# Optimization experiments

Measured on AMD Instinct MI355X. Metric: run time of the kernel, lower is better.

The kernel has to match this reference:

```python
import jax, jax.numpy as jnp
import numpy as np

SR = 44100
S_TAUS = [10.0, 50.0, 100.0]   # ms
L_TAUS = [500.0, 1500.0, 3000.0]  # ms
EPS = 1e-8


def ms2coef(ms, sr):
    return float(1.0 - np.exp(-2200.0 / (ms * sr)))


def ema(x, coef):
    # First-order leaky integrator y[t] = coef*x[t] + (1-coef)*y[t-1], y[-1]=0.
    # x: [B, T]; scan over time with carry of shape [B].
    coef = jnp.asarray(coef, x.dtype)
    one_m = jnp.asarray(1.0, x.dtype) - coef

    def step(carry, xt):
        y = coef * xt + one_m * carry
        return y, y

    _, ys = jax.lax.scan(step, jnp.zeros(x.shape[0], x.dtype), x.T)
    return ys.T  # [B, T]


def hadamard(x):
    # mid/side transform on channel dim (-2), orthonormal scaling
    m = x[..., 0, :] + x[..., 1, :]
    s = x[..., 0, :] - x[..., 1, :]
    return jnp.stack([m, s], axis=-2) * jnp.asarray(np.sqrt(0.5), x.dtype)


def ldr_feat(x_sq, s_coef, l_coef, shift):
    # log short-term envelope minus (time-aligned) log long-term envelope
    short = jnp.log(ema(x_sq, s_coef))
    long_ = jnp.log(ema(x_sq, l_coef))
    return short - jnp.roll(long_, -shift, axis=-1)


def setup_inputs() -> dict:
    key = jax.random.key(0)
    k1, k2 = jax.random.split(key)
    x_pred = jax.random.normal(k1, (4, 2, 1048576), dtype=jnp.float32)
    x_true = jax.random.normal(k2, (4, 2, 1048576), dtype=jnp.float32)
    return {"x_pred": x_pred, "x_true": x_true}


def reference(x_pred, x_true):
    xp = hadamard(x_pred)
    xt = hadamard(x_true)
    T = xp.shape[-1]
    ps = jnp.clip(jnp.square(xp), EPS, None).reshape(-1, T)
    ts = jnp.clip(jnp.square(xt), EPS, None).reshape(-1, T)
    total = jnp.asarray(0.0, x_pred.dtype)
    for s_ms, l_ms in zip(S_TAUS, L_TAUS):
        sc = ms2coef(s_ms, SR)
        lc = ms2coef(l_ms, SR)
        shift = int(SR * (l_ms - s_ms) * 0.0005)
        fp = ldr_feat(ps, sc, lc, shift)
        ft = ldr_feat(ts, sc, lc, shift)
        total = total + jnp.mean(jnp.abs(fp - ft))
    return total
```

## Files before the change

### kernel.cpp

```cpp
#include <hip/hip_runtime.h>
#include <cmath>


#define T_LEN    1048576
#define CHUNKS   256
#define CLEN     4096
#define NT1      256
#define SEG1     16
#define COLS     65536
#define JMAX     65535
#define EPS_CLIP 1e-8f
#define K2SEG    32
#define K2NSEG   8

struct K1Args {
  float d[6];
  float apw[6][7];
};
struct K2Args {
  float dL[6];
  float dL32[6];
};
struct CarryPack {
  float d[3];
  float apw[3][9];
};

__device__ __constant__ const int D_SHIFT[3] = {10804, 31972, 63945};

__global__ __launch_bounds__(NT1)
void k1_stage(const float* __restrict__ xp, const float* __restrict__ xt,
              float* __restrict__ Eloc, float* __restrict__ Bs,
              float* __restrict__ Bl, int mode, K1Args ka)
{
  int chunk = blockIdx.x, b = blockIdx.y;
  int which = b >> 2, sig = b & 3, tid = threadIdx.x;
  long base = (long)chunk * CLEN + (long)tid * SEG1;
  const float* x0 = (which ? xt : xp) + (long)sig * 2 * T_LEN;
  const float* x1 = x0 + T_LEN;

  float S[12];
#pragma unroll
  for (int j = 0; j < 12; j++) S[j] = 0.f;

#pragma unroll
  for (int i = 0; i < SEG1 / 4; i++) {
    float4 a = *(const float4*)(x0 + base + 4*i);
    float4 c4 = *(const float4*)(x1 + base + 4*i);
    float sm, sp, pm, ps;
#define STEP(CMP) \
    sm = a.CMP + c4.CMP; sp = a.CMP - c4.CMP; \
    pm = fmaxf(0.5f * sm * sm, EPS_CLIP); ps = fmaxf(0.5f * sp * sp, EPS_CLIP); \
    _Pragma("unroll") \
    for (int cf = 0; cf < 6; cf++) { \
      S[cf*2+0] = fmaf(ka.d[cf], S[cf*2+0], pm); \
      S[cf*2+1] = fmaf(ka.d[cf], S[cf*2+1], ps); \
    }
    STEP(x) STEP(y) STEP(z) STEP(w)
#undef STEP
  }

  int lane = tid & 63, w = tid >> 6;
#pragma unroll
  for (int i = 0; i < 6; i++) {
#pragma unroll
    for (int j = 0; j < 12; j++) {
      float up = __shfl_up(S[j], 1u << i, 64);
      if (lane >= (1 << i)) S[j] = fmaf(ka.apw[j >> 1][i], up, S[j]);
    }
  }
  __shared__ float WT[4][12];
  if (lane == 63)
#pragma unroll
    for (int j = 0; j < 12; j++) WT[w][j] = S[j];
  __syncthreads();
  float C[12];
#pragma unroll
  for (int j = 0; j < 12; j++) C[j] = 0.f;
#pragma unroll
  for (int i = 0; i < 4; i++) {
    if (i < w) {
#pragma unroll
      for (int j = 0; j < 12; j++)
        C[j] = fmaf(ka.apw[j >> 1][6], C[j], WT[i][j]);
    }
  }
  float alp[6];
#pragma unroll
  for (int cf = 0; cf < 6; cf++) {
    int e = lane + 1;
    float a = 1.f;
#pragma unroll
    for (int i = 0; i < 7; i++)
      if (e & (1 << i)) a *= ka.apw[cf][i];
    alp[cf] = a;
  }
#pragma unroll
  for (int j = 0; j < 12; j++) S[j] = fmaf(alp[j >> 1], C[j], S[j]);

  long col = (long)chunk * (CLEN / SEG1) + tid;
  if (mode & 2) {
#pragma unroll
    for (int k = 0; k < 3; k++)
#pragma unroll
      for (int st2 = 0; st2 < 2; st2++)
        Bs[(long)(4*k + which*2 + st2) * (4L*COLS) + (long)sig*COLS + col] = S[4*k + st2];
  }
  if (mode & 1) {
#pragma unroll
    for (int k = 0; k < 3; k++)
#pragma unroll
      for (int st2 = 0; st2 < 2; st2++)
        Bl[(long)(4*k + which*2 + st2) * (4L*COLS) + (long)sig*COLS + col] = S[4*k + 2 + st2];
  }
  if (mode != 2 && tid == NT1 - 1) {
#pragma unroll
    for (int cf = 0; cf < 6; cf++)
#pragma unroll
      for (int st = 0; st < 2; st++)
        Eloc[chunk * 96 + (which*8 + sig*2 + st) * 6 + cf] = S[cf*2 + st];
  }
}

__global__ __launch_bounds__(768)
void k2_scan(const float* __restrict__ Eloc, float* __restrict__ Y, K2Args ka,
             float* __restrict__ out)
{
  int col = threadIdx.x;
  int seg = threadIdx.y;
  if (col == 0 && seg == 0) out[0] = 0.f;
  float dL = ka.dL[col % 6];
  float A  = ka.dL32[col % 6];
  int c0 = seg * K2SEG;

  float yloc[K2SEG];
  float y = 0.f;
#pragma unroll
  for (int i = 0; i < K2SEG; i++) {
    y = fmaf(dL, y, Eloc[(c0 + i) * 96 + col]);
    yloc[i] = y;
  }
  __shared__ float SY[K2NSEG][96];
  SY[seg][col] = y;
  __syncthreads();
  float C = 0.f;
  for (int s = 0; s < seg; s++) C = fmaf(A, C, SY[s][col]);
  float w = dL;
#pragma unroll
  for (int i = 0; i < K2SEG; i++) {
    Y[(c0 + i) * 96 + col] = fmaf(w, C, yloc[i]);
    w *= dL;
  }
}

__global__ __launch_bounds__(256)
void k3_table(const float* __restrict__ Bl, const float* __restrict__ Y,
              float* __restrict__ Etab, CarryPack cp)
{
  int chunk = blockIdx.x, sig = blockIdx.y, tid = threadIdx.x;
  long col = (long)chunk * 256 + tid;

  float Yc[12];
#pragma unroll
  for (int j = 0; j < 12; j++) Yc[j] = 0.f;
  if (chunk > 0) {
    const float* Yp = Y + (chunk - 1) * 96;
    int rm = sig * 2;
#pragma unroll
    for (int k = 0; k < 3; k++) {
      int cf = 2*k + 1;
      Yc[4*k+0] = Yp[rm*6 + cf];       Yc[4*k+1] = Yp[(rm+1)*6 + cf];
      Yc[4*k+2] = Yp[(8+rm)*6 + cf];   Yc[4*k+3] = Yp[(8+rm+1)*6 + cf];
    }
  }
  float fac[3];
#pragma unroll
  for (int k = 0; k < 3; k++) {
    int e = tid + 1;
    float a = 1.f;
#pragma unroll
    for (int i = 0; i < 9; i++)
      if (e & (1 << i)) a *= cp.apw[k][i];
    fac[k] = a;
  }
#pragma unroll
  for (int k = 0; k < 3; k++) {
    float y0 = fmaf(fac[k], Yc[4*k+0], Bl[(long)(4*k+0)*(4L*COLS) + (long)sig*COLS + col]);
    float y1 = fmaf(fac[k], Yc[4*k+1], Bl[(long)(4*k+1)*(4L*COLS) + (long)sig*COLS + col]);
    float y2 = fmaf(fac[k], Yc[4*k+2], Bl[(long)(4*k+2)*(4L*COLS) + (long)sig*COLS + col]);
    float y3 = fmaf(fac[k], Yc[4*k+3], Bl[(long)(4*k+3)*(4L*COLS) + (long)sig*COLS + col]);
    float em = __log2f(y0) - __log2f(y2);
    float es = __log2f(y1) - __log2f(y3);
    long rowm = (long)(k*8 + sig*2);
    Etab[rowm * COLS + col] = em;
    Etab[(rowm+1) * COLS + col] = es;
  }
}

__device__ __forceinline__ float slow_lerp(const float* __restrict__ row, int q)
{
  int qm = q - 15;
  if (qm < 0) return row[0];
  int j = qm >> 4;
  if (j >= JMAX) return row[JMAX];
  float f = (float)(qm & 15) * 0.0625f;
  float a = row[j], b = row[j + 1];
  return fmaf(f, b - a, a);
}

__global__ __launch_bounds__(256)
void k4all(const float* __restrict__ xp, const float* __restrict__ xt,
           const float* __restrict__ Y, const float* __restrict__ Bs,
           const float* __restrict__ Etab, CarryPack cp, float* __restrict__ out)
{
  int chunk = blockIdx.x, sig = blockIdx.y, tid = threadIdx.x;
  long col = (long)chunk * 256 + tid;
  long base = col * 16;

  float Yc[12];
#pragma unroll
  for (int j = 0; j < 12; j++) Yc[j] = 0.f;
  if (chunk > 0) {
    const float* Yp = Y + (chunk - 1) * 96;
    int rm = sig * 2;
#pragma unroll
    for (int k = 0; k < 3; k++) {
      int cf = 2*k;
      Yc[4*k+0] = Yp[rm*6 + cf];       Yc[4*k+1] = Yp[(rm+1)*6 + cf];
      Yc[4*k+2] = Yp[(8+rm)*6 + cf];   Yc[4*k+3] = Yp[(8+rm+1)*6 + cf];
    }
  }
  float y[12];
  if (tid == 0) {
#pragma unroll
    for (int j = 0; j < 12; j++) y[j] = Yc[j];
  } else {
    float fac[3];
#pragma unroll
    for (int k = 0; k < 3; k++) {
      float a = 1.f;
#pragma unroll
      for (int i = 0; i < 8; i++)
        if (tid & (1 << i)) a *= cp.apw[k][i];
      fac[k] = a;
    }
#pragma unroll
    for (int k = 0; k < 3; k++)
#pragma unroll
      for (int q = 0; q < 4; q++)
        y[4*k+q] = fmaf(fac[k], Yc[4*k+q],
                        Bs[(long)(4*k+q)*(4L*COLS) + (long)sig*COLS + (col-1)]);
  }

  float tm0[3], tm1[3], tm2[3], ts0[3], ts1[3], ts2[3];
  int ofs[3], q0a[3]; bool fastp[3];
#pragma unroll
  for (int k = 0; k < 3; k++) {
    int q0 = (int)base + D_SHIFT[k]; if (q0 >= T_LEN) q0 -= T_LEN;
    q0a[k] = q0;
    int qm = q0 - 15;
    bool f = (qm >= 0) && ((qm >> 4) <= JMAX - 2);
    fastp[k] = f;
    const float* Tm = Etab + (long)(k * 8 + sig * 2) * COLS;
    const float* Ts = Tm + COLS;
    int j0 = f ? (qm >> 4) : 0;
    ofs[k] = f ? (qm & 15) : 0;
    tm0[k] = Tm[j0]; tm1[k] = Tm[j0 + 1]; tm2[k] = Tm[j0 + 2];
    ts0[k] = Ts[j0]; ts1[k] = Ts[j0 + 1]; ts2[k] = Ts[j0 + 2];
  }

  const float* p0 = xp + (long)sig * 2 * T_LEN;
  const float* p1 = p0 + T_LEN;
  const float* t0 = xt + (long)sig * 2 * T_LEN;
  const float* t1 = t0 + T_LEN;

  float acc0 = 0.f, acc1 = 0.f;
#pragma unroll
  for (int qt = 0; qt < 4; qt++) {
    float4 a4 = *(const float4*)(p0 + base + 4*qt);
    float4 b4 = *(const float4*)(p1 + base + 4*qt);
    float4 u4 = *(const float4*)(t0 + base + 4*qt);
    float4 w4 = *(const float4*)(t1 + base + 4*qt);
#define SAMP(CI, CMP) { \
      const int m = 4*qt + CI; \
      float sm = a4.CMP + b4.CMP, sd = a4.CMP - b4.CMP; \
      float pm = fmaxf(0.5f*sm*sm, EPS_CLIP), ps = fmaxf(0.5f*sd*sd, EPS_CLIP); \
      float em_ = u4.CMP + w4.CMP, ed_ = u4.CMP - w4.CMP; \
      float qm_ = fmaxf(0.5f*em_*em_, EPS_CLIP), qs_ = fmaxf(0.5f*ed_*ed_, EPS_CLIP); \
      _Pragma("unroll") \
      for (int k = 0; k < 3; k++) { \
        float dd = cp.d[k]; \
        y[4*k+0] = fmaf(dd, y[4*k+0], pm);  y[4*k+1] = fmaf(dd, y[4*k+1], ps); \
        y[4*k+2] = fmaf(dd, y[4*k+2], qm_); y[4*k+3] = fmaf(dd, y[4*k+3], qs_); \
        float Dm = __log2f(y[4*k+0]) - __log2f(y[4*k+2]); \
        float Ds = __log2f(y[4*k+1]) - __log2f(y[4*k+3]); \
        float em, es; \
        if (fastp[k]) { \
          int d0 = ofs[k] + m; \
          bool hi = d0 >= 16; \
          float am = hi ? tm1[k] : tm0[k], bm = hi ? tm2[k] : tm1[k]; \
          float as = hi ? ts1[k] : ts0[k], bs = hi ? ts2[k] : ts1[k]; \
          float f = (float)(d0 - (hi ? 16 : 0)) * 0.0625f; \
          em = fmaf(f, bm - am, am); \
          es = fmaf(f, bs - as, as); \
        } else { \
          int q = q0a[k] + m; if (q >= T_LEN) q -= T_LEN; \
          const float* Tm = Etab + (long)(k * 8 + sig * 2) * COLS; \
          em = slow_lerp(Tm, q); \
          es = slow_lerp(Tm + COLS, q); \
        } \
        acc0 += fabsf(Dm - em); \
        acc1 += fabsf(Ds - es); \
      } \
    }
    SAMP(0,x) SAMP(1,y) SAMP(2,z) SAMP(3,w)
#undef SAMP
  }

  float acc = acc0 + acc1;
#pragma unroll
  for (int off = 32; off > 0; off >>= 1) acc += __shfl_down(acc, off, 64);
  __shared__ float psum[4];
  int lane = tid & 63, w = tid >> 6;
  if (lane == 0) psum[w] = acc;
  __syncthreads();
  if (tid == 0) {
    const float SCALE = (float)(0.6931471805599453 / (8.0 * 1048576.0));
    float s = psum[0] + psum[1] + psum[2] + psum[3];
    atomicAdd(out, s * SCALE);
  }
}

extern "C" void kernel_launch(void* const* d_in, const int* in_sizes, int n_in,
                              void* d_out, int out_size, void* d_ws, size_t ws_size,
                              hipStream_t stream)
{
  (void)in_sizes; (void)n_in; (void)out_size;
  const float* xp = (const float*)d_in[0];
  const float* xt = (const float*)d_in[1];
  float* out = (float*)d_out;
  char* ws = (char*)d_ws;

  const size_t OFF_ELOC = 0;
  const size_t OFF_Y    = 98304;
  const size_t OFF_ETAB = 212992;
  const size_t OFF_B    = 6504448;
  const size_t HALF_B   = 12L * 4 * COLS * 4;
  const size_t NEED_FULL = OFF_B + 2 * HALF_B;
  float* Eloc = (float*)(ws + OFF_ELOC);
  float* Ybuf = (float*)(ws + OFF_Y);
  float* Etab = (float*)(ws + OFF_ETAB);
  float* Bsh  = (float*)(ws + OFF_B);
  float* Blo  = (float*)(ws + OFF_B + HALF_B);

  static const double S_MS[3] = {10.0, 50.0, 100.0};
  static const double L_MS[3] = {500.0, 1500.0, 3000.0};

  K1Args k1a; K2Args k2a; CarryPack cpS, cpL;
  for (int k = 0; k < 3; k++) {
    for (int which = 0; which < 2; which++) {
      int idx = 2 * k + which;
      double ms = which ? L_MS[k] : S_MS[k];
      float cF = (float)(1.0 - std::exp(-2200.0 / (ms * 44100.0)));
      float dF = 1.0f - cF;
      k1a.d[idx] = dF;
      double a16 = std::pow((double)dF, 16.0);
      for (int i = 0; i < 7; i++)
        k1a.apw[idx][i] = (float)std::pow(a16, (double)(1 << i));
      k2a.dL[idx]   = (float)std::pow((double)dF, (double)CLEN);
      k2a.dL32[idx] = (float)std::pow((double)dF, (double)CLEN * (double)K2SEG);
      CarryPack& cp = which ? cpL : cpS;
      cp.d[k] = dF;
      for (int i = 0; i < 9; i++)
        cp.apw[k][i] = (float)std::pow(a16, (double)(1 << i));
    }
  }

  bool full = (ws_size >= NEED_FULL);
  if (full) {
    k1_stage<<<dim3(CHUNKS, 8), NT1, 0, stream>>>(xp, xt, Eloc, Bsh, Blo, 3, k1a);
    k2_scan<<<dim3(1), dim3(96, K2NSEG), 0, stream>>>(Eloc, Ybuf, k2a, out);
    k3_table<<<dim3(CHUNKS, 4), 256, 0, stream>>>(Blo, Ybuf, Etab, cpL);
    k4all<<<dim3(CHUNKS, 4), 256, 0, stream>>>(xp, xt, Ybuf, Bsh, Etab, cpS, out);
  } else {
    k1_stage<<<dim3(CHUNKS, 8), NT1, 0, stream>>>(xp, xt, Eloc, Bsh, Bsh, 1, k1a);
    k2_scan<<<dim3(1), dim3(96, K2NSEG), 0, stream>>>(Eloc, Ybuf, k2a, out);
    k3_table<<<dim3(CHUNKS, 4), 256, 0, stream>>>(Bsh, Ybuf, Etab, cpL);
    k1_stage<<<dim3(CHUNKS, 8), NT1, 0, stream>>>(xp, xt, Eloc, Bsh, Bsh, 2, k1a);
    k4all<<<dim3(CHUNKS, 4), 256, 0, stream>>>(xp, xt, Ybuf, Bsh, Etab, cpS, out);
  }
}
```

Before: 139.7 us.

## Split final k4all pass across the three tau pairs via grid z dimension

The final fused pass now launches a third grid dimension, one block slice per short/long tau pair, instead of one thread handling all three pairs. Each thread keeps 4 EMA states and one interpolation table window instead of 12 and 3, which cuts register pressure and triples the number of blocks (1024 to 3072) to raise occupancy. In exchange, every input sample is read three times from global memory (likely served by L2/cache) and the squaring and clipping work is repeated per pair.

```diff
diff --git a/kernel.cpp b/kernel.cpp
--- a/kernel.cpp
+++ b/kernel.cpp
@@ -213,66 +213,47 @@
            const float* __restrict__ Y, const float* __restrict__ Bs,
            const float* __restrict__ Etab, CarryPack cp, float* __restrict__ out)
 {
-  int chunk = blockIdx.x, sig = blockIdx.y, tid = threadIdx.x;
+  int chunk = blockIdx.x, sig = blockIdx.y, ks = blockIdx.z, tid = threadIdx.x;
   long col = (long)chunk * 256 + tid;
   long base = col * 16;
 
-  float Yc[12];
-#pragma unroll
-  for (int j = 0; j < 12; j++) Yc[j] = 0.f;
+  float Yc0 = 0.f, Yc1 = 0.f, Yc2 = 0.f, Yc3 = 0.f;
   if (chunk > 0) {
     const float* Yp = Y + (chunk - 1) * 96;
-    int rm = sig * 2;
-#pragma unroll
-    for (int k = 0; k < 3; k++) {
-      int cf = 2*k;
-      Yc[4*k+0] = Yp[rm*6 + cf];       Yc[4*k+1] = Yp[(rm+1)*6 + cf];
-      Yc[4*k+2] = Yp[(8+rm)*6 + cf];   Yc[4*k+3] = Yp[(8+rm+1)*6 + cf];
-    }
-  }
-  float y[12];
+    int rm = sig * 2, cf = 2 * ks;
+    Yc0 = Yp[rm*6 + cf];       Yc1 = Yp[(rm+1)*6 + cf];
+    Yc2 = Yp[(8+rm)*6 + cf];   Yc3 = Yp[(8+rm+1)*6 + cf];
+  }
+  float y0, y1, y2, y3;
   if (tid == 0) {
-#pragma unroll
-    for (int j = 0; j < 12; j++) y[j] = Yc[j];
+    y0 = Yc0; y1 = Yc1; y2 = Yc2; y3 = Yc3;
   } else {
-    float fac[3];
-#pragma unroll
-    for (int k = 0; k < 3; k++) {
-      float a = 1.f;
-#pragma unroll
-      for (int i = 0; i < 8; i++)
-        if (tid & (1 << i)) a *= cp.apw[k][i];
-      fac[k] = a;
-    }
-#pragma unroll
-    for (int k = 0; k < 3; k++)
-#pragma unroll
-      for (int q = 0; q < 4; q++)
-        y[4*k+q] = fmaf(fac[k], Yc[4*k+q],
-                        Bs[(long)(4*k+q)*(4L*COLS) + (long)sig*COLS + (col-1)]);
-  }
-
-  float tm0[3], tm1[3], tm2[3], ts0[3], ts1[3], ts2[3];
-  int ofs[3], q0a[3]; bool fastp[3];
-#pragma unroll
-  for (int k = 0; k < 3; k++) {
-    int q0 = (int)base + D_SHIFT[k]; if (q0 >= T_LEN) q0 -= T_LEN;
-    q0a[k] = q0;
-    int qm = q0 - 15;
-    bool f = (qm >= 0) && ((qm >> 4) <= JMAX - 2);
-    fastp[k] = f;
-    const float* Tm = Etab + (long)(k * 8 + sig * 2) * COLS;
-    const float* Ts = Tm + COLS;
-    int j0 = f ? (qm >> 4) : 0;
-    ofs[k] = f ? (qm & 15) : 0;
-    tm0[k] = Tm[j0]; tm1[k] = Tm[j0 + 1]; tm2[k] = Tm[j0 + 2];
-    ts0[k] = Ts[j0]; ts1[k] = Ts[j0 + 1]; ts2[k] = Ts[j0 + 2];
-  }
+    float a = 1.f;
+#pragma unroll
+    for (int i = 0; i < 8; i++)
+      if (tid & (1 << i)) a *= cp.apw[ks][i];
+    long pc = (long)sig * COLS + (col - 1);
+    y0 = fmaf(a, Yc0, Bs[(long)(4*ks+0)*(4L*COLS) + pc]);
+    y1 = fmaf(a, Yc1, Bs[(long)(4*ks+1)*(4L*COLS) + pc]);
+    y2 = fmaf(a, Yc2, Bs[(long)(4*ks+2)*(4L*COLS) + pc]);
+    y3 = fmaf(a, Yc3, Bs[(long)(4*ks+3)*(4L*COLS) + pc]);
+  }
+
+  const float* Tm = Etab + (long)(ks * 8 + sig * 2) * COLS;
+  const float* Ts = Tm + COLS;
+  int q0 = (int)base + D_SHIFT[ks]; if (q0 >= T_LEN) q0 -= T_LEN;
+  int qm0 = q0 - 15;
+  bool fastp = (qm0 >= 0) && ((qm0 >> 4) <= JMAX - 2);
+  int j0 = fastp ? (qm0 >> 4) : 0;
+  int ofs = fastp ? (qm0 & 15) : 0;
+  float tm0 = Tm[j0], tm1 = Tm[j0 + 1], tm2 = Tm[j0 + 2];
+  float ts0 = Ts[j0], ts1 = Ts[j0 + 1], ts2 = Ts[j0 + 2];
 
   const float* p0 = xp + (long)sig * 2 * T_LEN;
   const float* p1 = p0 + T_LEN;
   const float* t0 = xt + (long)sig * 2 * T_LEN;
   const float* t1 = t0 + T_LEN;
+  float dd = cp.d[ks];
 
   float acc0 = 0.f, acc1 = 0.f;
 #pragma unroll
@@ -287,31 +268,26 @@
       float pm = fmaxf(0.5f*sm*sm, EPS_CLIP), ps = fmaxf(0.5f*sd*sd, EPS_CLIP); \
       float em_ = u4.CMP + w4.CMP, ed_ = u4.CMP - w4.CMP; \
       float qm_ = fmaxf(0.5f*em_*em_, EPS_CLIP), qs_ = fmaxf(0.5f*ed_*ed_, EPS_CLIP); \
-      _Pragma("unroll") \
-      for (int k = 0; k < 3; k++) { \
-        float dd = cp.d[k]; \
-        y[4*k+0] = fmaf(dd, y[4*k+0], pm);  y[4*k+1] = fmaf(dd, y[4*k+1], ps); \
-        y[4*k+2] = fmaf(dd, y[4*k+2], qm_); y[4*k+3] = fmaf(dd, y[4*k+3], qs_); \
-        float Dm = __log2f(y[4*k+0]) - __log2f(y[4*k+2]); \
-        float Ds = __log2f(y[4*k+1]) - __log2f(y[4*k+3]); \
-        float em, es; \
-        if (fastp[k]) { \
-          int d0 = ofs[k] + m; \
-          bool hi = d0 >= 16; \
-          float am = hi ? tm1[k] : tm0[k], bm = hi ? tm2[k] : tm1[k]; \
-          float as = hi ? ts1[k] : ts0[k], bs = hi ? ts2[k] : ts1[k]; \
-          float f = (float)(d0 - (hi ? 16 : 0)) * 0.0625f; \
-          em = fmaf(f, bm - am, am); \
-          es = fmaf(f, bs - as, as); \
-        } else { \
-          int q = q0a[k] + m; if (q >= T_LEN) q -= T_LEN; \
-          const float* Tm = Etab + (long)(k * 8 + sig * 2) * COLS; \
-          em = slow_lerp(Tm, q); \
-          es = slow_lerp(Tm + COLS, q); \
-        } \
-        acc0 += fabsf(Dm - em); \
-        acc1 += fabsf(Ds - es); \
+      y0 = fmaf(dd, y0, pm);  y1 = fmaf(dd, y1, ps); \
+      y2 = fmaf(dd, y2, qm_); y3 = fmaf(dd, y3, qs_); \
+      float Dm = __log2f(y0) - __log2f(y2); \
+      float Ds = __log2f(y1) - __log2f(y3); \
+      float em, es; \
+      if (fastp) { \
+        int d0 = ofs + m; \
+        bool hi = d0 >= 16; \
+        float am = hi ? tm1 : tm0, bm = hi ? tm2 : tm1; \
+        float as = hi ? ts1 : ts0, bs = hi ? ts2 : ts1; \
+        float f = (float)(d0 - (hi ? 16 : 0)) * 0.0625f; \
+        em = fmaf(f, bm - am, am); \
+        es = fmaf(f, bs - as, as); \
+      } else { \
+        int q = q0 + m; if (q >= T_LEN) q -= T_LEN; \
+        em = slow_lerp(Tm, q); \
+        es = slow_lerp(Ts, q); \
       } \
+      acc0 += fabsf(Dm - em); \
+      acc1 += fabsf(Ds - es); \
     }
     SAMP(0,x) SAMP(1,y) SAMP(2,z) SAMP(3,w)
 #undef SAMP
@@ -381,12 +357,12 @@
     k1_stage<<<dim3(CHUNKS, 8), NT1, 0, stream>>>(xp, xt, Eloc, Bsh, Blo, 3, k1a);
     k2_scan<<<dim3(1), dim3(96, K2NSEG), 0, stream>>>(Eloc, Ybuf, k2a, out);
     k3_table<<<dim3(CHUNKS, 4), 256, 0, stream>>>(Blo, Ybuf, Etab, cpL);
-    k4all<<<dim3(CHUNKS, 4), 256, 0, stream>>>(xp, xt, Ybuf, Bsh, Etab, cpS, out);
+    k4all<<<dim3(CHUNKS, 4, 3), 256, 0, stream>>>(xp, xt, Ybuf, Bsh, Etab, cpS, out);
   } else {
     k1_stage<<<dim3(CHUNKS, 8), NT1, 0, stream>>>(xp, xt, Eloc, Bsh, Bsh, 1, k1a);
     k2_scan<<<dim3(1), dim3(96, K2NSEG), 0, stream>>>(Eloc, Ybuf, k2a, out);
     k3_table<<<dim3(CHUNKS, 4), 256, 0, stream>>>(Bsh, Ybuf, Etab, cpL);
     k1_stage<<<dim3(CHUNKS, 8), NT1, 0, stream>>>(xp, xt, Eloc, Bsh, Bsh, 2, k1a);
-    k4all<<<dim3(CHUNKS, 4), 256, 0, stream>>>(xp, xt, Ybuf, Bsh, Etab, cpS, out);
-  }
-}
+    k4all<<<dim3(CHUNKS, 4, 3), 256, 0, stream>>>(xp, xt, Ybuf, Bsh, Etab, cpS, out);
+  }
+}
```

Result: slower. 167.6 us (+20.0%).

## Split k4all work across thread pairs for pred and true signals

Applied to the files above, without the earlier changes.

Each column of 16 samples is now handled by two threads, one for the predicted signal and one for the true signal. They exchange log-envelope values with a lane shuffle, and each thread computes one of the two mid/side error terms. The kernel launches 512 threads per block instead of 256, which halves per-thread registers and serial work and raises parallelism across the 1024 blocks. The cost is an extra shuffle per sample and coefficient, plus less coalesced loads, since paired threads read different arrays at the same offset.

```diff
diff --git a/kernel.cpp b/kernel.cpp
--- a/kernel.cpp
+++ b/kernel.cpp
@@ -208,32 +208,33 @@
   return fmaf(f, b - a, a);
 }
 
-__global__ __launch_bounds__(256)
+__global__ __launch_bounds__(512)
 void k4all(const float* __restrict__ xp, const float* __restrict__ xt,
            const float* __restrict__ Y, const float* __restrict__ Bs,
            const float* __restrict__ Etab, CarryPack cp, float* __restrict__ out)
 {
   int chunk = blockIdx.x, sig = blockIdx.y, tid = threadIdx.x;
-  long col = (long)chunk * 256 + tid;
+  int cl = tid >> 1, role = tid & 1;
+  long col = (long)chunk * 256 + cl;
   long base = col * 16;
 
-  float Yc[12];
-#pragma unroll
-  for (int j = 0; j < 12; j++) Yc[j] = 0.f;
+  float Yc[6];
+#pragma unroll
+  for (int j = 0; j < 6; j++) Yc[j] = 0.f;
   if (chunk > 0) {
     const float* Yp = Y + (chunk - 1) * 96;
-    int rm = sig * 2;
+    int rm = sig * 2 + (role ? 8 : 0);
 #pragma unroll
     for (int k = 0; k < 3; k++) {
       int cf = 2*k;
-      Yc[4*k+0] = Yp[rm*6 + cf];       Yc[4*k+1] = Yp[(rm+1)*6 + cf];
-      Yc[4*k+2] = Yp[(8+rm)*6 + cf];   Yc[4*k+3] = Yp[(8+rm+1)*6 + cf];
-    }
-  }
-  float y[12];
-  if (tid == 0) {
-#pragma unroll
-    for (int j = 0; j < 12; j++) y[j] = Yc[j];
+      Yc[2*k+0] = Yp[rm*6 + cf];
+      Yc[2*k+1] = Yp[(rm+1)*6 + cf];
+    }
+  }
+  float y[6];
+  if (cl == 0) {
+#pragma unroll
+    for (int j = 0; j < 6; j++) y[j] = Yc[j];
   } else {
     float fac[3];
 #pragma unroll
@@ -241,92 +242,84 @@
       float a = 1.f;
 #pragma unroll
       for (int i = 0; i < 8; i++)
-        if (tid & (1 << i)) a *= cp.apw[k][i];
+        if (cl & (1 << i)) a *= cp.apw[k][i];
       fac[k] = a;
     }
-#pragma unroll
-    for (int k = 0; k < 3; k++)
-#pragma unroll
-      for (int q = 0; q < 4; q++)
-        y[4*k+q] = fmaf(fac[k], Yc[4*k+q],
-                        Bs[(long)(4*k+q)*(4L*COLS) + (long)sig*COLS + (col-1)]);
-  }
-
-  float tm0[3], tm1[3], tm2[3], ts0[3], ts1[3], ts2[3];
+    long pc = (long)sig * COLS + (col - 1);
+#pragma unroll
+    for (int k = 0; k < 3; k++) {
+      y[2*k+0] = fmaf(fac[k], Yc[2*k+0], Bs[(long)(4*k + 2*role + 0)*(4L*COLS) + pc]);
+      y[2*k+1] = fmaf(fac[k], Yc[2*k+1], Bs[(long)(4*k + 2*role + 1)*(4L*COLS) + pc]);
+    }
+  }
+
+  const float* Trow[3];
+  float t0[3], t1[3], t2[3];
   int ofs[3], q0a[3]; bool fastp[3];
 #pragma unroll
   for (int k = 0; k < 3; k++) {
     int q0 = (int)base + D_SHIFT[k]; if (q0 >= T_LEN) q0 -= T_LEN;
     q0a[k] = q0;
-    int qm = q0 - 15;
-    bool f = (qm >= 0) && ((qm >> 4) <= JMAX - 2);
+    int qm0 = q0 - 15;
+    bool f = (qm0 >= 0) && ((qm0 >> 4) <= JMAX - 2);
     fastp[k] = f;
-    const float* Tm = Etab + (long)(k * 8 + sig * 2) * COLS;
-    const float* Ts = Tm + COLS;
-    int j0 = f ? (qm >> 4) : 0;
-    ofs[k] = f ? (qm & 15) : 0;
-    tm0[k] = Tm[j0]; tm1[k] = Tm[j0 + 1]; tm2[k] = Tm[j0 + 2];
-    ts0[k] = Ts[j0]; ts1[k] = Ts[j0 + 1]; ts2[k] = Ts[j0 + 2];
-  }
-
-  const float* p0 = xp + (long)sig * 2 * T_LEN;
-  const float* p1 = p0 + T_LEN;
-  const float* t0 = xt + (long)sig * 2 * T_LEN;
-  const float* t1 = t0 + T_LEN;
-
-  float acc0 = 0.f, acc1 = 0.f;
+    Trow[k] = Etab + (long)(k * 8 + sig * 2 + role) * COLS;
+    int j0 = f ? (qm0 >> 4) : 0;
+    ofs[k] = f ? (qm0 & 15) : 0;
+    t0[k] = Trow[k][j0]; t1[k] = Trow[k][j0 + 1]; t2[k] = Trow[k][j0 + 2];
+  }
+
+  const float* xA = (role ? xt : xp) + (long)sig * 2 * T_LEN;
+  const float* xB = xA + T_LEN;
+
+  float acc = 0.f;
 #pragma unroll
   for (int qt = 0; qt < 4; qt++) {
-    float4 a4 = *(const float4*)(p0 + base + 4*qt);
-    float4 b4 = *(const float4*)(p1 + base + 4*qt);
-    float4 u4 = *(const float4*)(t0 + base + 4*qt);
-    float4 w4 = *(const float4*)(t1 + base + 4*qt);
+    float4 a4 = *(const float4*)(xA + base + 4*qt);
+    float4 b4 = *(const float4*)(xB + base + 4*qt);
 #define SAMP(CI, CMP) { \
       const int m = 4*qt + CI; \
-      float sm = a4.CMP + b4.CMP, sd = a4.CMP - b4.CMP; \
-      float pm = fmaxf(0.5f*sm*sm, EPS_CLIP), ps = fmaxf(0.5f*sd*sd, EPS_CLIP); \
-      float em_ = u4.CMP + w4.CMP, ed_ = u4.CMP - w4.CMP; \
-      float qm_ = fmaxf(0.5f*em_*em_, EPS_CLIP), qs_ = fmaxf(0.5f*ed_*ed_, EPS_CLIP); \
+      float s1 = a4.CMP + b4.CMP, s2 = a4.CMP - b4.CMP; \
+      float p0 = fmaxf(0.5f*s1*s1, EPS_CLIP), p1 = fmaxf(0.5f*s2*s2, EPS_CLIP); \
       _Pragma("unroll") \
       for (int k = 0; k < 3; k++) { \
         float dd = cp.d[k]; \
-        y[4*k+0] = fmaf(dd, y[4*k+0], pm);  y[4*k+1] = fmaf(dd, y[4*k+1], ps); \
-        y[4*k+2] = fmaf(dd, y[4*k+2], qm_); y[4*k+3] = fmaf(dd, y[4*k+3], qs_); \
-        float Dm = __log2f(y[4*k+0]) - __log2f(y[4*k+2]); \
-        float Ds = __log2f(y[4*k+1]) - __log2f(y[4*k+3]); \
-        float em, es; \
+        y[2*k+0] = fmaf(dd, y[2*k+0], p0); \
+        y[2*k+1] = fmaf(dd, y[2*k+1], p1); \
+        float lg0 = __log2f(y[2*k+0]); \
+        float lg1 = __log2f(y[2*k+1]); \
+        float send = role ? lg0 : lg1; \
+        float recv = __shfl_xor(send, 1, 64); \
+        float diff = role ? (recv - lg1) : (lg0 - recv); \
+        float Ev; \
         if (fastp[k]) { \
           int d0 = ofs[k] + m; \
           bool hi = d0 >= 16; \
-          float am = hi ? tm1[k] : tm0[k], bm = hi ? tm2[k] : tm1[k]; \
-          float as = hi ? ts1[k] : ts0[k], bs = hi ? ts2[k] : ts1[k]; \
+          float fa = hi ? t1[k] : t0[k], fb = hi ? t2[k] : t1[k]; \
           float f = (float)(d0 - (hi ? 16 : 0)) * 0.0625f; \
-          em = fmaf(f, bm - am, am); \
-          es = fmaf(f, bs - as, as); \
+          Ev = fmaf(f, fb - fa, fa); \
         } else { \
           int q = q0a[k] + m; if (q >= T_LEN) q -= T_LEN; \
-          const float* Tm = Etab + (long)(k * 8 + sig * 2) * COLS; \
-          em = slow_lerp(Tm, q); \
-          es = slow_lerp(Tm + COLS, q); \
+          Ev = slow_lerp(Trow[k], q); \
         } \
-        acc0 += fabsf(Dm - em); \
-        acc1 += fabsf(Ds - es); \
+        acc += fabsf(diff - Ev); \
       } \
     }
     SAMP(0,x) SAMP(1,y) SAMP(2,z) SAMP(3,w)
 #undef SAMP
   }
 
-  float acc = acc0 + acc1;
 #pragma unroll
   for (int off = 32; off > 0; off >>= 1) acc += __shfl_down(acc, off, 64);
-  __shared__ float psum[4];
+  __shared__ float psum[8];
   int lane = tid & 63, w = tid >> 6;
   if (lane == 0) psum[w] = acc;
   __syncthreads();
   if (tid == 0) {
     const float SCALE = (float)(0.6931471805599453 / (8.0 * 1048576.0));
-    float s = psum[0] + psum[1] + psum[2] + psum[3];
+    float s = 0.f;
+#pragma unroll
+    for (int i = 0; i < 8; i++) s += psum[i];
     atomicAdd(out, s * SCALE);
   }
 }
@@ -381,12 +374,12 @@
     k1_stage<<<dim3(CHUNKS, 8), NT1, 0, stream>>>(xp, xt, Eloc, Bsh, Blo, 3, k1a);
     k2_scan<<<dim3(1), dim3(96, K2NSEG), 0, stream>>>(Eloc, Ybuf, k2a, out);
     k3_table<<<dim3(CHUNKS, 4), 256, 0, stream>>>(Blo, Ybuf, Etab, cpL);
-    k4all<<<dim3(CHUNKS, 4), 256, 0, stream>>>(xp, xt, Ybuf, Bsh, Etab, cpS, out);
+    k4all<<<dim3(CHUNKS, 4), 512, 0, stream>>>(xp, xt, Ybuf, Bsh, Etab, cpS, out);
   } else {
     k1_stage<<<dim3(CHUNKS, 8), NT1, 0, stream>>>(xp, xt, Eloc, Bsh, Bsh, 1, k1a);
     k2_scan<<<dim3(1), dim3(96, K2NSEG), 0, stream>>>(Eloc, Ybuf, k2a, out);
     k3_table<<<dim3(CHUNKS, 4), 256, 0, stream>>>(Bsh, Ybuf, Etab, cpL);
     k1_stage<<<dim3(CHUNKS, 8), NT1, 0, stream>>>(xp, xt, Eloc, Bsh, Bsh, 2, k1a);
-    k4all<<<dim3(CHUNKS, 4), 256, 0, stream>>>(xp, xt, Ybuf, Bsh, Etab, cpS, out);
-  }
-}
+    k4all<<<dim3(CHUNKS, 4), 512, 0, stream>>>(xp, xt, Ybuf, Bsh, Etab, cpS, out);
+  }
+}
```

Result: slower. 147.0 us (+5.2%).
